# Kernel tuning notes

Measured on AMD Instinct MI355X. Metric: run time of the kernel, lower is better.

## Reference

```python
import jax, jax.numpy as jnp
import numpy as np

N, D_IN, D_OUT, N_CLASSES = 4096, 1024, 256, 64


def setup_inputs() -> dict:
    key = jax.random.key(0)
    k1, k2, k3, k4 = jax.random.split(key, 4)
    x = jax.random.normal(k1, (N, D_IN), dtype=jnp.float32)
    W = jax.random.normal(k2, (D_IN, D_OUT), dtype=jnp.float32) * 0.02
    b = jax.random.normal(k3, (D_OUT,), dtype=jnp.float32) * 0.02
    targets = jax.random.randint(k4, (N,), 0, N_CLASSES, dtype=jnp.int64)
    return {"x": x, "W": W, "b": b, "targets": targets}


def reference(x, W, b, targets):
    # FC projection (activation = 'linear')
    h = jnp.matmul(x, W) + b                      # [N, d]
    # Pairwise euclidean distances D[i, j] = ||h_i - h_j||_2, matching
    # tf.norm(tf.abs(anchor - others), axis=1) in the original per-anchor loop.
    sq = jnp.sum(h * h, axis=1)                   # [N]
    d2 = sq[:, None] + sq[None, :] - 2.0 * jnp.matmul(h, h.T)
    dist = jnp.sqrt(jnp.maximum(d2, 0.0))         # [N, N]
    same = targets[:, None] == targets[None, :]   # class_division mask
    inf = jnp.float32(np.inf)
    # Hardest positive: max distance among same-class (includes self at 0,
    hardest_pos = jnp.max(jnp.where(same, dist, -inf), axis=1)  # [N]
    # Hardest negative: min distance among different-class samples.
    hardest_neg = jnp.min(jnp.where(same, inf, dist), axis=1)   # [N]
    loss = jnp.sum(jnp.log1p(jnp.exp(hardest_pos - hardest_neg)))
    return loss
```

## Files before the change

### kernel.cpp

```cpp
#include <hip/hip_runtime.h>
#include <math.h>

#define NROWS 4096
#define DIN   1024
#define DOUT  256
#define NJB   64
#define NPAIR 528

using bfrag = __attribute__((ext_vector_type(8))) short;
using ffrag = __attribute__((ext_vector_type(4))) float;


static __device__ __forceinline__ unsigned short f2bf(float f) {
    unsigned int u = __float_as_uint(f);
    u = (u + 0x7fffu + ((u >> 16) & 1u)) >> 16;
    return (unsigned short)u;
}
static __device__ __forceinline__ unsigned int pack2(float lo, float hi) {
    return (unsigned int)f2bf(lo) | ((unsigned int)f2bf(hi) << 16);
}

__global__ __launch_bounds__(256) void setup(const float* __restrict__ W,
                                             unsigned short* __restrict__ Ws,
                                             float* __restrict__ sq,
                                             float* __restrict__ out) {
    const int f = blockIdx.x * 256 + threadIdx.x;
    {
        const int l  = f & 63;
        const int ks = (f >> 6) & 31;
        const int nt = f >> 11;
        const int col = nt * 16 + (l & 15);
        const int k0  = ks * 32 + (l >> 4) * 8;
        float a[8];
#pragma unroll
        for (int j = 0; j < 8; ++j) a[j] = W[(size_t)(k0 + j) * DOUT + col];
        uint4 v;
        v.x = pack2(a[0], a[1]);
        v.y = pack2(a[2], a[3]);
        v.z = pack2(a[4], a[5]);
        v.w = pack2(a[6], a[7]);
        *(uint4*)&Ws[(size_t)f * 8] = v;
    }
    if (f < NROWS) sq[f] = 0.0f;
    if (f == 0) *out = 0.0f;
}

__global__ __launch_bounds__(256) void gemm1_direct(
    const float* __restrict__ x, const unsigned short* __restrict__ Ws,
    const float* __restrict__ b,
    unsigned short* __restrict__ hs, float* __restrict__ sq) {
    __shared__ __align__(16) short Axs[32 * 528];
    __shared__ __align__(16) short T[4][16][36];

    const int tid = threadIdx.x;
    const int w   = tid >> 6;
    const int l   = tid & 63;
    const int m16 = l & 15;
    const int q   = l >> 4;
    const int t   = blockIdx.x >> 1;
    const int h   = blockIdx.x & 1;

    const int r  = tid >> 4;
    const int cc = tid & 15;
    const float* xrow = x + (size_t)(t * 16 + r) * DIN;
#pragma unroll
    for (int s = 0; s < 8; ++s) {
        const int c = s * 128 + cc * 8;
        const float4 p0 = *(const float4*)(xrow + c);
        const float4 p1 = *(const float4*)(xrow + c + 4);
        uint4 v;
        v.x = pack2(p0.x, p0.y);
        v.y = pack2(p0.z, p0.w);
        v.z = pack2(p1.x, p1.y);
        v.w = pack2(p1.z, p1.w);
        const int ks = c >> 5;
        const int lw = ((c >> 3) & 3) * 16 + r;
        *(uint4*)&Axs[ks * 528 + lw * 8] = v;
    }
    __syncthreads();

    const int nt0 = h * 8 + w * 2;
    const bfrag* B0 = (const bfrag*)Ws + ((size_t)nt0 * 32) * 64 + l;
    const bfrag* B1 = (const bfrag*)Ws + ((size_t)(nt0 + 1) * 32) * 64 + l;

    ffrag acc0 = {}, acc1 = {};
#pragma unroll
    for (int ks = 0; ks < 32; ++ks) {
        const bfrag a = *(const bfrag*)&Axs[ks * 528 + l * 8];
        acc0 = __builtin_amdgcn_mfma_f32_16x16x32_bf16(a, B0[ks * 64], acc0, 0, 0, 0);
        acc1 = __builtin_amdgcn_mfma_f32_16x16x32_bf16(a, B1[ks * 64], acc1, 0, 0, 0);
    }

    const float bc0 = b[nt0 * 16 + m16];
    const float bc1 = b[(nt0 + 1) * 16 + m16];
    float hv0[4], hv1[4];
#pragma unroll
    for (int reg = 0; reg < 4; ++reg) {
        hv0[reg] = acc0[reg] + bc0;
        hv1[reg] = acc1[reg] + bc1;
    }

#pragma unroll
    for (int reg = 0; reg < 4; ++reg) {
        float p = hv0[reg] * hv0[reg] + hv1[reg] * hv1[reg];
#pragma unroll
        for (int mask = 1; mask < 16; mask <<= 1) p += __shfl_xor(p, mask);
        if (m16 == 0) atomicAdd(&sq[t * 16 + q * 4 + reg], p);
    }

#pragma unroll
    for (int reg = 0; reg < 4; ++reg) {
        T[w][q * 4 + reg][m16]      = f2bf(hv0[reg]);
        T[w][q * 4 + reg][16 + m16] = f2bf(hv1[reg]);
    }
    const int ksH = h * 4 + w;
    bfrag v = *(const bfrag*)&T[w][m16][q * 8];
    ((bfrag*)hs)[((size_t)t * 8 + ksH) * 64 + l] = v;
}

__global__ __launch_bounds__(256) void hardest_tri(
    const unsigned short* __restrict__ hs, const float* __restrict__ sq,
    const int* __restrict__ targets,
    float* __restrict__ pmax, float* __restrict__ pmin) {
    const int tid = threadIdx.x;
    const int w   = tid >> 6;
    const int wi  = w & 1, wj = w >> 1;
    const int l   = tid & 63;
    const int m16 = l & 15;
    const int q   = l >> 4;

    const int k = blockIdx.x;
    int bj = (int)((sqrtf(8.0f * (float)k + 1.0f) - 1.0f) * 0.5f);
    while ((bj + 1) * (bj + 2) / 2 <= k) ++bj;
    while (bj * (bj + 1) / 2 > k) --bj;
    const int bi = k - bj * (bj + 1) / 2;
    const bool diag = (bi == bj);

    const int iw = bi * 128 + wi * 64;
    const int jw = bj * 128 + wj * 64;
    const int tA = iw >> 4;
    const int tB = jw >> 4;

    ffrag acc[4][4] = {};

#pragma unroll
    for (int ks = 0; ks < 8; ++ks) {
        bfrag a[4], bb[4];
#pragma unroll
        for (int mi = 0; mi < 4; ++mi)
            a[mi] = *(const bfrag*)&hs[(((size_t)(tA + mi) * 8 + ks) * 64 + l) * 8];
#pragma unroll
        for (int nj = 0; nj < 4; ++nj)
            bb[nj] = *(const bfrag*)&hs[(((size_t)(tB + nj) * 8 + ks) * 64 + l) * 8];
#pragma unroll
        for (int mi = 0; mi < 4; ++mi)
#pragma unroll
            for (int nj = 0; nj < 4; ++nj)
                acc[mi][nj] = __builtin_amdgcn_mfma_f32_16x16x32_bf16(
                    a[mi], bb[nj], acc[mi][nj], 0, 0, 0);
    }

    int   tj[4];
    float svj[4];
#pragma unroll
    for (int nj = 0; nj < 4; ++nj) {
        const int col = jw + nj * 16 + m16;
        tj[nj]  = targets[col];
        svj[nj] = sq[col];
    }

    float cmx[4], cmn[4];
#pragma unroll
    for (int nj = 0; nj < 4; ++nj) { cmx[nj] = -INFINITY; cmn[nj] = INFINITY; }

    const int jblk = bj * 2 + wj;
#pragma unroll
    for (int mi = 0; mi < 4; ++mi)
#pragma unroll
        for (int reg = 0; reg < 4; ++reg) {
            const int row = iw + mi * 16 + q * 4 + reg;
            const int ti  = targets[row];
            const float si = sq[row];
            float mx = -INFINITY, mn = INFINITY;
#pragma unroll
            for (int nj = 0; nj < 4; ++nj) {
                const float g    = acc[mi][nj][reg];
                const float vrow = fmaf(-2.0f, g, svj[nj]);
                const float vcol = fmaf(-2.0f, g, si);
                if (tj[nj] == ti) {
                    mx = fmaxf(mx, vrow);
                    cmx[nj] = fmaxf(cmx[nj], vcol);
                } else {
                    mn = fminf(mn, vrow);
                    cmn[nj] = fminf(cmn[nj], vcol);
                }
            }
#pragma unroll
            for (int mask = 1; mask < 16; mask <<= 1) {
                mx = fmaxf(mx, __shfl_xor(mx, mask));
                mn = fminf(mn, __shfl_xor(mn, mask));
            }
            if (m16 == 0) {
                pmax[(size_t)jblk * NROWS + row] = mx;
                pmin[(size_t)jblk * NROWS + row] = mn;
            }
        }

    if (!diag) {
        const int iblk = bi * 2 + wi;
#pragma unroll
        for (int nj = 0; nj < 4; ++nj) {
            float mx = cmx[nj], mn = cmn[nj];
            mx = fmaxf(mx, __shfl_xor(mx, 16));
            mn = fminf(mn, __shfl_xor(mn, 16));
            mx = fmaxf(mx, __shfl_xor(mx, 32));
            mn = fminf(mn, __shfl_xor(mn, 32));
            if (q == 0) {
                const int col = jw + nj * 16 + m16;
                pmax[(size_t)iblk * NROWS + col] = mx;
                pmin[(size_t)iblk * NROWS + col] = mn;
            }
        }
    }
}

__global__ __launch_bounds__(256) void finalize(const float* __restrict__ sq,
                                                const float* __restrict__ pmax,
                                                const float* __restrict__ pmin,
                                                float* __restrict__ out) {
    __shared__ float wsum[4];
    const int i = blockIdx.x * 256 + threadIdx.x;
    float mp = -INFINITY, mn = INFINITY;
#pragma unroll
    for (int c = 0; c < NJB; ++c) {
        mp = fmaxf(mp, pmax[c * NROWS + i]);
        mn = fminf(mn, pmin[c * NROWS + i]);
    }
    const float si = sq[i];
    const float hp = sqrtf(fmaxf(si + mp, 0.0f));
    const float hn = sqrtf(fmaxf(si + mn, 0.0f));
    const float d  = hp - hn;
    float li = fmaxf(d, 0.0f) + log1pf(expf(-fabsf(d)));
#pragma unroll
    for (int off = 32; off; off >>= 1) li += __shfl_down(li, off);
    const int lane = threadIdx.x & 63, wv = threadIdx.x >> 6;
    if (lane == 0) wsum[wv] = li;
    __syncthreads();
    if (threadIdx.x == 0)
        atomicAdd(out, wsum[0] + wsum[1] + wsum[2] + wsum[3]);
}

extern "C" void kernel_launch(void* const* d_in, const int* in_sizes, int n_in,
                              void* d_out, int out_size, void* d_ws, size_t ws_size,
                              hipStream_t stream) {
    const float* x       = (const float*)d_in[0];
    const float* W       = (const float*)d_in[1];
    const float* b       = (const float*)d_in[2];
    const int*   targets = (const int*)d_in[3];
    float* out = (float*)d_out;

    unsigned short* Ws   = (unsigned short*)d_ws;
    unsigned short* hs   = Ws + DOUT * DIN;
    float*          sq   = (float*)(hs + NROWS * DOUT);
    float*          pmax = sq + NROWS;
    float*          pmin = pmax + NJB * NROWS;

    setup<<<16 * 32 * 64 / 256, 256, 0, stream>>>(W, Ws, sq, out);
    gemm1_direct<<<NROWS / 16 * 2, 256, 0, stream>>>(x, Ws, b, hs, sq);
    hardest_tri<<<NPAIR, 256, 0, stream>>>(hs, sq, targets, pmax, pmin);
    finalize<<<NROWS / 256, 256, 0, stream>>>(sq, pmax, pmin, out);
}
```

Before: 116.9 us.

## Replace per-block partial min/max arrays with atomic order-preserving keys; widen gemm1 blocks

The hardest-pair kernel now reduces row and column max/min directly into per-row unsigned keys using atomicMax/atomicMin on an order-preserving float encoding. The finalize kernel no longer has to scan 64 partial arrays per row. The setup kernel initializes these keys. Separately, the projection GEMM uses 512-thread blocks covering all 256 output columns per 16-row tile, so each x tile is loaded and converted once instead of twice. The atomics add contention on shared rows, and the larger blocks change occupancy.

```diff
diff --git a/kernel.cpp b/kernel.cpp
--- a/kernel.cpp
+++ b/kernel.cpp
@@ -4,7 +4,6 @@
 #define NROWS 4096
 #define DIN   1024
 #define DOUT  256
-#define NJB   64
 #define NPAIR 528
 
 using bfrag = __attribute__((ext_vector_type(8))) short;
@@ -19,10 +18,19 @@
 static __device__ __forceinline__ unsigned int pack2(float lo, float hi) {
     return (unsigned int)f2bf(lo) | ((unsigned int)f2bf(hi) << 16);
 }
+static __device__ __forceinline__ unsigned int fkey(float f) {
+    unsigned int b = __float_as_uint(f);
+    return (b & 0x80000000u) ? ~b : (b | 0x80000000u);
+}
+static __device__ __forceinline__ float funkey(unsigned int u) {
+    return __uint_as_float((u & 0x80000000u) ? (u & 0x7fffffffu) : ~u);
+}
 
 __global__ __launch_bounds__(256) void setup(const float* __restrict__ W,
                                              unsigned short* __restrict__ Ws,
                                              float* __restrict__ sq,
+                                             unsigned int* __restrict__ pmaxk,
+                                             unsigned int* __restrict__ pmink,
                                              float* __restrict__ out) {
     const int f = blockIdx.x * 256 + threadIdx.x;
     {
@@ -41,31 +49,34 @@
         v.w = pack2(a[6], a[7]);
         *(uint4*)&Ws[(size_t)f * 8] = v;
     }
-    if (f < NROWS) sq[f] = 0.0f;
+    if (f < NROWS) {
+        sq[f]    = 0.0f;
+        pmaxk[f] = 0u;
+        pmink[f] = 0xFFFFFFFFu;
+    }
     if (f == 0) *out = 0.0f;
 }
 
-__global__ __launch_bounds__(256) void gemm1_direct(
+__global__ __launch_bounds__(512) void gemm1_direct(
     const float* __restrict__ x, const unsigned short* __restrict__ Ws,
     const float* __restrict__ b,
     unsigned short* __restrict__ hs, float* __restrict__ sq) {
     __shared__ __align__(16) short Axs[32 * 528];
-    __shared__ __align__(16) short T[4][16][36];
+    __shared__ __align__(16) short T[8][16][36];
 
     const int tid = threadIdx.x;
     const int w   = tid >> 6;
     const int l   = tid & 63;
     const int m16 = l & 15;
     const int q   = l >> 4;
-    const int t   = blockIdx.x >> 1;
-    const int h   = blockIdx.x & 1;
-
-    const int r  = tid >> 4;
-    const int cc = tid & 15;
+    const int t   = blockIdx.x;
+
+    const int r  = tid >> 5;
+    const int cc = tid & 31;
     const float* xrow = x + (size_t)(t * 16 + r) * DIN;
 #pragma unroll
-    for (int s = 0; s < 8; ++s) {
-        const int c = s * 128 + cc * 8;
+    for (int s = 0; s < 4; ++s) {
+        const int c = s * 256 + cc * 8;
         const float4 p0 = *(const float4*)(xrow + c);
         const float4 p1 = *(const float4*)(xrow + c + 4);
         uint4 v;
@@ -79,7 +90,7 @@
     }
     __syncthreads();
 
-    const int nt0 = h * 8 + w * 2;
+    const int nt0 = w * 2;
     const bfrag* B0 = (const bfrag*)Ws + ((size_t)nt0 * 32) * 64 + l;
     const bfrag* B1 = (const bfrag*)Ws + ((size_t)(nt0 + 1) * 32) * 64 + l;
 
@@ -113,15 +124,14 @@
         T[w][q * 4 + reg][m16]      = f2bf(hv0[reg]);
         T[w][q * 4 + reg][16 + m16] = f2bf(hv1[reg]);
     }
-    const int ksH = h * 4 + w;
     bfrag v = *(const bfrag*)&T[w][m16][q * 8];
-    ((bfrag*)hs)[((size_t)t * 8 + ksH) * 64 + l] = v;
+    ((bfrag*)hs)[((size_t)t * 8 + w) * 64 + l] = v;
 }
 
 __global__ __launch_bounds__(256) void hardest_tri(
     const unsigned short* __restrict__ hs, const float* __restrict__ sq,
     const int* __restrict__ targets,
-    float* __restrict__ pmax, float* __restrict__ pmin) {
+    unsigned int* __restrict__ pmaxk, unsigned int* __restrict__ pmink) {
     const int tid = threadIdx.x;
     const int w   = tid >> 6;
     const int wi  = w & 1, wj = w >> 1;
@@ -173,7 +183,6 @@
 #pragma unroll
     for (int nj = 0; nj < 4; ++nj) { cmx[nj] = -INFINITY; cmn[nj] = INFINITY; }
 
-    const int jblk = bj * 2 + wj;
 #pragma unroll
     for (int mi = 0; mi < 4; ++mi)
 #pragma unroll
@@ -201,13 +210,12 @@
                 mn = fminf(mn, __shfl_xor(mn, mask));
             }
             if (m16 == 0) {
-                pmax[(size_t)jblk * NROWS + row] = mx;
-                pmin[(size_t)jblk * NROWS + row] = mn;
+                atomicMax(&pmaxk[row], fkey(mx));
+                atomicMin(&pmink[row], fkey(mn));
             }
         }
 
     if (!diag) {
-        const int iblk = bi * 2 + wi;
 #pragma unroll
         for (int nj = 0; nj < 4; ++nj) {
             float mx = cmx[nj], mn = cmn[nj];
@@ -217,25 +225,21 @@
             mn = fminf(mn, __shfl_xor(mn, 32));
             if (q == 0) {
                 const int col = jw + nj * 16 + m16;
-                pmax[(size_t)iblk * NROWS + col] = mx;
-                pmin[(size_t)iblk * NROWS + col] = mn;
+                atomicMax(&pmaxk[col], fkey(mx));
+                atomicMin(&pmink[col], fkey(mn));
             }
         }
     }
 }
 
 __global__ __launch_bounds__(256) void finalize(const float* __restrict__ sq,
-                                                const float* __restrict__ pmax,
-                                                const float* __restrict__ pmin,
+                                                const unsigned int* __restrict__ pmaxk,
+                                                const unsigned int* __restrict__ pmink,
                                                 float* __restrict__ out) {
     __shared__ float wsum[4];
     const int i = blockIdx.x * 256 + threadIdx.x;
-    float mp = -INFINITY, mn = INFINITY;
-#pragma unroll
-    for (int c = 0; c < NJB; ++c) {
-        mp = fmaxf(mp, pmax[c * NROWS + i]);
-        mn = fminf(mn, pmin[c * NROWS + i]);
-    }
+    const float mp = funkey(pmaxk[i]);
+    const float mn = funkey(pmink[i]);
     const float si = sq[i];
     const float hp = sqrtf(fmaxf(si + mp, 0.0f));
     const float hn = sqrtf(fmaxf(si + mn, 0.0f));
@@ -259,14 +263,14 @@
     const int*   targets = (const int*)d_in[3];
     float* out = (float*)d_out;
 
-    unsigned short* Ws   = (unsigned short*)d_ws;
-    unsigned short* hs   = Ws + DOUT * DIN;
-    float*          sq   = (float*)(hs + NROWS * DOUT);
-    float*          pmax = sq + NROWS;
-    float*          pmin = pmax + NJB * NROWS;
-
-    setup<<<16 * 32 * 64 / 256, 256, 0, stream>>>(W, Ws, sq, out);
-    gemm1_direct<<<NROWS / 16 * 2, 256, 0, stream>>>(x, Ws, b, hs, sq);
-    hardest_tri<<<NPAIR, 256, 0, stream>>>(hs, sq, targets, pmax, pmin);
-    finalize<<<NROWS / 256, 256, 0, stream>>>(sq, pmax, pmin, out);
-}
+    unsigned short* Ws    = (unsigned short*)d_ws;
+    unsigned short* hs    = Ws + DOUT * DIN;
+    float*          sq    = (float*)(hs + NROWS * DOUT);
+    unsigned int*   pmaxk = (unsigned int*)(sq + NROWS);
+    unsigned int*   pmink = pmaxk + NROWS;
+
+    setup<<<16 * 32 * 64 / 256, 256, 0, stream>>>(W, Ws, sq, pmaxk, pmink, out);
+    gemm1_direct<<<NROWS / 16, 512, 0, stream>>>(x, Ws, b, hs, sq);
+    hardest_tri<<<NPAIR, 256, 0, stream>>>(hs, sq, targets, pmaxk, pmink);
+    finalize<<<NROWS / 256, 256, 0, stream>>>(sq, pmaxk, pmink, out);
+}
```

New measurement: 99.03 us. 15.3% less time.
